# Performance work log

Measured on AMD Instinct MI355X. Metric: run time of the kernel, lower is better.

The kernel has to match this reference:

```python
import jax, jax.numpy as jnp
import numpy as np
import math

B, S, D, H = 2, 2048, 1024, 16
HD = D // H  # 64


def _rope(x, cos, sin):
    # x: [B,S,H,HD]; cos/sin: [S, HD//2]
    x2 = x.reshape(*x.shape[:-1], HD // 2, 2)
    x0, x1 = x2[..., 0], x2[..., 1]
    c = cos[None, :, None, :]
    s = sin[None, :, None, :]
    r0 = x0 * c - x1 * s
    r1 = x0 * s + x1 * c
    return jnp.stack([r0, r1], axis=-1).reshape(x.shape)


def setup_inputs() -> dict:
    key = jax.random.key(0)
    ks = jax.random.split(key, 6)
    x = jax.random.normal(ks[0], (B, S, D), dtype=jnp.float32)
    wq = jax.random.normal(ks[1], (D, D), dtype=jnp.float32) * 0.02
    wk = jax.random.normal(ks[2], (D, D), dtype=jnp.float32) * 0.02
    wv = jax.random.normal(ks[3], (D, D), dtype=jnp.float32) * 0.02
    wo = jax.random.normal(ks[4], (D, D), dtype=jnp.float32) * 0.02
    # standard RoPE frequencies: theta = 10000^(-2i/HD)
    inv_freq = 1.0 / (10000.0 ** (jnp.arange(0, HD, 2, dtype=jnp.float32) / HD))
    t = jnp.arange(S, dtype=jnp.float32)
    ang = t[:, None] * inv_freq[None, :]  # [S, HD//2]
    freqs_cos = jnp.cos(ang)
    freqs_sin = jnp.sin(ang)
    # causal additive mask [S, S]
    mask = jnp.where(jnp.tril(jnp.ones((S, S), dtype=bool)), 0.0, -1e9).astype(jnp.float32)
    return {"x": x, "wq": wq, "wk": wk, "wv": wv, "wo": wo,
            "freqs_cos": freqs_cos, "freqs_sin": freqs_sin, "mask": mask}


def reference(x, wq, wk, wv, wo, freqs_cos, freqs_sin, mask):
    b, s, d = x.shape
    # nn.Linear with no bias: y = x @ W^T
    q = jnp.einsum('bsd,od->bso', x, wq).reshape(b, s, H, HD)
    k = jnp.einsum('bsd,od->bso', x, wk).reshape(b, s, H, HD)
    v = jnp.einsum('bsd,od->bso', x, wv).reshape(b, s, H, HD)
    q = _rope(q, freqs_cos, freqs_sin)
    k = _rope(k, freqs_cos, freqs_sin)
    # [B,H,S,HD]
    q = q.transpose(0, 2, 1, 3)
    k = k.transpose(0, 2, 1, 3)
    v = v.transpose(0, 2, 1, 3)
    scores = jnp.einsum('bhqd,bhkd->bhqk', q, k) / math.sqrt(HD)
    scores = scores + mask[None, None, :, :]
    p = jax.nn.softmax(scores.astype(jnp.float32), axis=-1).astype(q.dtype)
    out = jnp.einsum('bhqk,bhkd->bhqd', p, v)
    out = out.transpose(0, 2, 1, 3).reshape(b, s, d)
    return jnp.einsum('bsd,od->bso', out, wo)
```

## Files before the change

### kernel.cpp

```cpp
#include <hip/hip_runtime.h>
#include <hip/hip_bf16.h>
#include <stdint.h>

#define NB 2
#define NS 2048
#define ND 1024
#define NH 16
#define NM (NB*NS)

typedef __attribute__((ext_vector_type(8))) short bf16x8;
typedef __attribute__((ext_vector_type(4))) float f32x4;

static __device__ __forceinline__ f32x4 mfma16(bf16x8 a, bf16x8 b, f32x4 c) {
  return __builtin_amdgcn_mfma_f32_16x16x32_bf16(a, b, c, 0, 0, 0);
}

static __device__ __forceinline__ void gload_lds16(const void* g, void* l) {
  __builtin_amdgcn_global_load_lds(
      (const __attribute__((address_space(1))) void*)g,
      (__attribute__((address_space(3))) void*)l, 16, 0, 0);
}

static __device__ __forceinline__ uint32_t pkbf2(float a, float b) {
  return (uint32_t)__bfloat16_as_ushort(__float2bfloat16(a)) |
         ((uint32_t)__bfloat16_as_ushort(__float2bfloat16(b)) << 16);
}

#define QSCALE 0.18033688011112042f

struct alignas(8) bh4 { __hip_bfloat16 x, y, z, w; };

__global__ void cvt_all(const float* __restrict__ x,
                        const float* __restrict__ w0, const float* __restrict__ w1,
                        const float* __restrict__ w2, const float* __restrict__ w3,
                        __hip_bfloat16* xb, __hip_bfloat16* o0, __hip_bfloat16* o1,
                        __hip_bfloat16* o2, __hip_bfloat16* o3) {
  const int b = blockIdx.x;
  const float* in;
  __hip_bfloat16* out;
  int i;
  if (b < 4096) { in = x; out = xb; i = b * 256 + threadIdx.x; }
  else {
    const int t = (b - 4096) >> 10;
    in  = (t == 0) ? w0 : (t == 1) ? w1 : (t == 2) ? w2 : w3;
    out = (t == 0) ? o0 : (t == 1) ? o1 : (t == 2) ? o2 : o3;
    i = ((b - 4096) & 1023) * 256 + threadIdx.x;
  }
  float4 v = reinterpret_cast<const float4*>(in)[i];
  bh4 o;
  o.x = __float2bfloat16(v.x);
  o.y = __float2bfloat16(v.y);
  o.z = __float2bfloat16(v.z);
  o.w = __float2bfloat16(v.w);
  reinterpret_cast<bh4*>(out)[i] = o;
}

__global__ __launch_bounds__(256) void gemm_qkv(
    const __hip_bfloat16* __restrict__ A,
    const __hip_bfloat16* __restrict__ Wq,
    const __hip_bfloat16* __restrict__ Wk,
    const __hip_bfloat16* __restrict__ Wv,
    const float* __restrict__ fcos,
    const float* __restrict__ fsin,
    __hip_bfloat16* __restrict__ Qo,
    __hip_bfloat16* __restrict__ Ko,
    __hip_bfloat16* __restrict__ Vo) {
  __shared__ __hip_bfloat16 sA[128 * 32];
  __shared__ __hip_bfloat16 sB[128 * 32];
  __shared__ __align__(16) char xtr[33792];

  const int wsel = blockIdx.y >> 3;
  const __hip_bfloat16* W = (wsel == 0) ? Wq : (wsel == 1) ? Wk : Wv;

  const int tid = threadIdx.x;
  const int wid = tid >> 6;
  const int lane = tid & 63;
  const int l4 = lane >> 4, l16 = lane & 15;
  const int brow = blockIdx.x * 128;
  const int bcol = (blockIdx.y & 7) * 128;
  const int wr = (wid >> 1) * 64;
  const int wc = (wid & 1) * 64;
  const int ss0 = brow & 2047;
  const int bbb = brow >> 11;

  if (wsel < 2) {
    float2* tab = (float2*)xtr;
#pragma unroll
    for (int i = 0; i < 4; ++i) {
      const int e = i * 1024 + tid * 4;
      const int ssl = e >> 5, p = e & 31;
      float4 c4 = *(const float4*)&fcos[(ss0 + ssl) * 32 + p];
      float4 s4 = *(const float4*)&fsin[(ss0 + ssl) * 32 + p];
      tab[ssl * 33 + p + 0] = {c4.x, s4.x};
      tab[ssl * 33 + p + 1] = {c4.y, s4.y};
      tab[ssl * 33 + p + 2] = {c4.z, s4.z};
      tab[ssl * 33 + p + 3] = {c4.w, s4.w};
    }
  }

  f32x4 acc[4][4] = {};

  const __hip_bfloat16* Ap = A + (size_t)(brow + (tid >> 2)) * 1024 + (tid & 3) * 8;
  const __hip_bfloat16* Wp = W + (size_t)(bcol + (tid >> 2)) * 1024 + (tid & 3) * 8;
  char* sAc = (char*)sA + wid * 1024;
  char* sBc = (char*)sB + wid * 1024;

  for (int kt = 0; kt < 32; ++kt) {
    const int k0 = kt * 32;
    __syncthreads();
    gload_lds16(Ap + k0,             sAc);
    gload_lds16(Ap + 64 * 1024 + k0, sAc + 4096);
    gload_lds16(Wp + k0,             sBc);
    gload_lds16(Wp + 64 * 1024 + k0, sBc + 4096);
    __syncthreads();

    bf16x8 af[4], bfr[4];
#pragma unroll
    for (int i = 0; i < 4; ++i)
      af[i] = *(const bf16x8*)&sA[(wr + i * 16 + l16) * 32 + l4 * 8];
#pragma unroll
    for (int i = 0; i < 4; ++i)
      bfr[i] = *(const bf16x8*)&sB[(wc + i * 16 + l16) * 32 + l4 * 8];
#pragma unroll
    for (int mi = 0; mi < 4; ++mi)
#pragma unroll
      for (int ni = 0; ni < 4; ++ni)
        acc[mi][ni] = mfma16(af[mi], bfr[ni], acc[mi][ni]);
  }

  if (wsel == 2) {
    __hip_bfloat16 (*tt)[132] = (__hip_bfloat16(*)[132])xtr;
#pragma unroll
    for (int h = 0; h < 2; ++h) {
      __syncthreads();
      if ((wid & 1) == h) {
#pragma unroll
        for (int mi = 0; mi < 4; ++mi)
#pragma unroll
          for (int ni = 0; ni < 4; ++ni) {
            const int c = ni * 16 + l16;
            const int r0 = wr + mi * 16 + l4 * 4;
            uint2 w;
            w.x = pkbf2(acc[mi][ni][0], acc[mi][ni][1]);
            w.y = pkbf2(acc[mi][ni][2], acc[mi][ni][3]);
            *(uint2*)&tt[c][r0] = w;
          }
      }
      __syncthreads();
      const int cl = tid >> 2;
      const int rq = (tid & 3) * 32;
      const int o = bcol + h * 64 + cl;
      const int hh = o >> 6, hd = o & 63;
      __hip_bfloat16* dst =
          Vo + ((size_t)(bbb * 16 + hh) * 64 + hd) * 2048 + ss0 + rq;
#pragma unroll
      for (int k2 = 0; k2 < 4; ++k2)
        *(uint4*)&dst[k2 * 8] = *(const uint4*)&tt[cl][rq + k2 * 8];
    }
  } else {
    const float2* tab = (const float2*)xtr;
    __hip_bfloat16* dst = (wsel == 0) ? Qo : Ko;
#pragma unroll
    for (int mi = 0; mi < 4; ++mi)
#pragma unroll
      for (int ni = 0; ni < 4; ++ni)
#pragma unroll
        for (int j = 0; j < 4; ++j) {
          float v = acc[mi][ni][j];
          const int rloc = wr + mi * 16 + l4 * 4 + j;
          const int col = bcol + wc + ni * 16 + l16;
          const int hh = col >> 6, hd = col & 63;
          float other = __shfl_xor(v, 1);
          const float2 cs = tab[rloc * 33 + (hd >> 1)];
          float r = (col & 1) ? (other * cs.y + v * cs.x)
                              : (v * cs.x - other * cs.y);
          if (wsel == 0) r *= QSCALE;
          dst[((size_t)(bbb * 16 + hh) * 2048 + ss0 + rloc) * 64 + hd] =
              __float2bfloat16(r);
        }
  }
}

__global__ __launch_bounds__(256) void gemm_out(
    const __hip_bfloat16* __restrict__ A,
    const __hip_bfloat16* __restrict__ W,
    float* __restrict__ C) {
  __shared__ __hip_bfloat16 sA[64 * 32];
  __shared__ __hip_bfloat16 sB[128 * 32];

  const int tid = threadIdx.x;
  const int wid = tid >> 6;
  const int lane = tid & 63;
  const int l4 = lane >> 4, l16 = lane & 15;
  const int brow = blockIdx.x * 64;
  const int bcol = blockIdx.y * 128;
  const int wr = (wid & 1) * 32;
  const int wc = (wid >> 1) * 64;

  f32x4 acc[2][4] = {};

  const __hip_bfloat16* Ap = A + (size_t)(brow + (tid >> 2)) * 1024 + (tid & 3) * 8;
  const __hip_bfloat16* Wp = W + (size_t)(bcol + (tid >> 2)) * 1024 + (tid & 3) * 8;
  char* sAc = (char*)sA + wid * 1024;
  char* sBc = (char*)sB + wid * 1024;

  for (int kt = 0; kt < 32; ++kt) {
    const int k0 = kt * 32;
    __syncthreads();
    gload_lds16(Ap + k0,             sAc);
    gload_lds16(Wp + k0,             sBc);
    gload_lds16(Wp + 64 * 1024 + k0, sBc + 4096);
    __syncthreads();

    bf16x8 af[2], bfr[4];
#pragma unroll
    for (int i = 0; i < 2; ++i)
      af[i] = *(const bf16x8*)&sA[(wr + i * 16 + l16) * 32 + l4 * 8];
#pragma unroll
    for (int i = 0; i < 4; ++i)
      bfr[i] = *(const bf16x8*)&sB[(wc + i * 16 + l16) * 32 + l4 * 8];
#pragma unroll
    for (int mi = 0; mi < 2; ++mi)
#pragma unroll
      for (int ni = 0; ni < 4; ++ni)
        acc[mi][ni] = mfma16(af[mi], bfr[ni], acc[mi][ni]);
  }

#pragma unroll
  for (int mi = 0; mi < 2; ++mi)
#pragma unroll
    for (int ni = 0; ni < 4; ++ni)
#pragma unroll
      for (int j = 0; j < 4; ++j) {
        const int row = brow + wr + mi * 16 + l4 * 4 + j;
        const int col = bcol + wc + ni * 16 + l16;
        C[(size_t)row * 1024 + col] = acc[mi][ni][j];
      }
}

__global__ __launch_bounds__(256) void attn_fwd(
    const __hip_bfloat16* __restrict__ Q,
    const __hip_bfloat16* __restrict__ K,
    const __hip_bfloat16* __restrict__ VT,
    __hip_bfloat16* __restrict__ AO) {
  const int L = blockIdx.x;
  int qt, bh;
  if (L < 256) { qt = 15 - (L >> 5); bh = L & 31; }
  else         { qt = (L >> 5) - 8;  bh = L & 31; }
  const int bb = bh >> 4;
  const int hh = bh & 15;
  const int tid = threadIdx.x;
  const int wid = tid >> 6;
  const int lane = tid & 63;
  const int l4 = lane >> 4, l16 = lane & 15;
  const int wq0 = qt * 128 + wid * 32;

  const __hip_bfloat16* Qg = Q + (size_t)bh * 2048 * 64;
  const __hip_bfloat16* Kg = K + (size_t)bh * 2048 * 64;
  const __hip_bfloat16* Vg = VT + (size_t)bh * 64 * 2048;

  __shared__ __hip_bfloat16 sP[4][32][72];

  bf16x8 qf[2][2];
#pragma unroll
  for (int q2 = 0; q2 < 2; ++q2)
#pragma unroll
    for (int dk = 0; dk < 2; ++dk)
      qf[q2][dk] = *(const bf16x8*)&Qg[(size_t)(wq0 + q2 * 16 + l16) * 64 + dk * 32 + l4 * 8];

  float lrun[2] = {0.f, 0.f};
  f32x4 oacc[2][4] = {};

  const int lastkv = (wq0 + 31) >> 6;
  for (int kv = 0; kv <= lastkv; ++kv) {
    const int kb = kv * 64;

    bf16x8 kfr[4][2];
#pragma unroll
    for (int kf = 0; kf < 4; ++kf)
#pragma unroll
      for (int dk = 0; dk < 2; ++dk)
        kfr[kf][dk] = *(const bf16x8*)&Kg[(size_t)(kb + kf * 16 + l16) * 64 + dk * 32 + l4 * 8];

    f32x4 sacc[4][2] = {};
    __builtin_amdgcn_s_setprio(1);
#pragma unroll
    for (int dk = 0; dk < 2; ++dk)
#pragma unroll
      for (int kf = 0; kf < 4; ++kf)
#pragma unroll
        for (int q2 = 0; q2 < 2; ++q2)
          sacc[kf][q2] = mfma16(kfr[kf][dk], qf[q2][dk], sacc[kf][q2]);
    __builtin_amdgcn_s_setprio(0);

    bf16x8 vfr[4][2];
#pragma unroll
    for (int df = 0; df < 4; ++df)
#pragma unroll
      for (int ks = 0; ks < 2; ++ks)
        vfr[df][ks] = *(const bf16x8*)&Vg[(size_t)(df * 16 + l16) * 2048 + kb + ks * 32 + l4 * 8];

    const bool need_mask = (kb + 63 > wq0);
#pragma unroll
    for (int q2 = 0; q2 < 2; ++q2) {
      const int qi = wq0 + q2 * 16 + l16;
      float pe[16];
#pragma unroll
      for (int kf = 0; kf < 4; ++kf)
#pragma unroll
        for (int j = 0; j < 4; ++j) {
          float s = sacc[kf][q2][j];
          if (need_mask && (kb + kf * 16 + l4 * 4 + j > qi)) s = -1e30f;
          pe[kf * 4 + j] = exp2f(s);
        }
#pragma unroll
      for (int kf = 0; kf < 4; ++kf) {
        uint2 w;
        w.x = pkbf2(pe[kf * 4 + 0], pe[kf * 4 + 1]);
        w.y = pkbf2(pe[kf * 4 + 2], pe[kf * 4 + 3]);
        *(uint2*)&sP[wid][q2 * 16 + l16][kf * 16 + l4 * 4] = w;
      }
      float ts = 0.f;
#pragma unroll
      for (int t = 0; t < 16; ++t) ts += pe[t];
      ts += __shfl_xor(ts, 16);
      ts += __shfl_xor(ts, 32);
      lrun[q2] += ts;
    }

    __builtin_amdgcn_s_setprio(1);
#pragma unroll
    for (int ks = 0; ks < 2; ++ks) {
      bf16x8 pfr[2];
#pragma unroll
      for (int mf = 0; mf < 2; ++mf)
        pfr[mf] = *(const bf16x8*)&sP[wid][mf * 16 + l16][ks * 32 + l4 * 8];
#pragma unroll
      for (int mf = 0; mf < 2; ++mf)
#pragma unroll
        for (int df = 0; df < 4; ++df)
          oacc[mf][df] = mfma16(pfr[mf], vfr[df][ks], oacc[mf][df]);
    }
    __builtin_amdgcn_s_setprio(0);
  }

  float inv[2];
#pragma unroll
  for (int q2 = 0; q2 < 2; ++q2) inv[q2] = 1.f / lrun[q2];
#pragma unroll
  for (int mf = 0; mf < 2; ++mf)
#pragma unroll
    for (int j = 0; j < 4; ++j) {
      const float ir = __shfl(inv[mf], l4 * 4 + j);
      const int ss = wq0 + mf * 16 + l4 * 4 + j;
#pragma unroll
      for (int df = 0; df < 4; ++df) {
        const int dd = hh * 64 + df * 16 + l16;
        AO[((size_t)bb * 2048 + ss) * 1024 + dd] =
            __float2bfloat16(oacc[mf][df][j] * ir);
      }
    }
}

extern "C" void kernel_launch(void* const* d_in, const int* in_sizes, int n_in,
                              void* d_out, int out_size, void* d_ws, size_t ws_size,
                              hipStream_t stream) {
  const float* x  = (const float*)d_in[0];
  const float* wq = (const float*)d_in[1];
  const float* wk = (const float*)d_in[2];
  const float* wv = (const float*)d_in[3];
  const float* wo = (const float*)d_in[4];
  const float* fc = (const float*)d_in[5];
  const float* fs = (const float*)d_in[6];

  char* ws = (char*)d_ws;
  const size_t MB = 1024 * 1024;
  __hip_bfloat16* xb  = (__hip_bfloat16*)(ws);
  __hip_bfloat16* wqb = (__hip_bfloat16*)(ws + 8 * MB);
  __hip_bfloat16* wkb = (__hip_bfloat16*)(ws + 10 * MB);
  __hip_bfloat16* wvb = (__hip_bfloat16*)(ws + 12 * MB);
  __hip_bfloat16* wob = (__hip_bfloat16*)(ws + 14 * MB);
  __hip_bfloat16* qws = (__hip_bfloat16*)(ws + 16 * MB);
  __hip_bfloat16* kws = (__hip_bfloat16*)(ws + 24 * MB);
  __hip_bfloat16* vws = (__hip_bfloat16*)(ws + 32 * MB);
  __hip_bfloat16* ao  = (__hip_bfloat16*)(ws + 40 * MB);

  cvt_all<<<8192, 256, 0, stream>>>(x, wq, wk, wv, wo, xb, wqb, wkb, wvb, wob);

  gemm_qkv<<<dim3(NM / 128, 24), 256, 0, stream>>>(xb, wqb, wkb, wvb, fc, fs,
                                                   qws, kws, vws);

  attn_fwd<<<dim3(512), 256, 0, stream>>>(qws, kws, vws, ao);

  gemm_out<<<dim3(NM / 64, ND / 128), 256, 0, stream>>>(ao, wob, (float*)d_out);
}
```

Before: 229.9 us.

## Double-buffer K/V tiles in LDS for attention and remap GEMM blocks across XCDs

```diff
diff --git a/kernel.cpp b/kernel.cpp
--- a/kernel.cpp
+++ b/kernel.cpp
@@ -69,15 +69,19 @@
   __shared__ __hip_bfloat16 sB[128 * 32];
   __shared__ __align__(16) char xtr[33792];
 
-  const int wsel = blockIdx.y >> 3;
+  const int bl = blockIdx.x;
+  const int logical = (bl & 7) * 96 + (bl >> 3);
+  const int xt = logical / 24;
+  const int yy = logical - xt * 24;
+  const int wsel = yy >> 3;
   const __hip_bfloat16* W = (wsel == 0) ? Wq : (wsel == 1) ? Wk : Wv;
 
   const int tid = threadIdx.x;
   const int wid = tid >> 6;
   const int lane = tid & 63;
   const int l4 = lane >> 4, l16 = lane & 15;
-  const int brow = blockIdx.x * 128;
-  const int bcol = (blockIdx.y & 7) * 128;
+  const int brow = xt * 128;
+  const int bcol = (yy & 7) * 128;
   const int wr = (wid >> 1) * 64;
   const int wc = (wid & 1) * 64;
   const int ss0 = brow & 2047;
@@ -188,12 +192,14 @@
   __shared__ __hip_bfloat16 sA[64 * 32];
   __shared__ __hip_bfloat16 sB[128 * 32];
 
+  const int bl = blockIdx.x;
+  const int logical = (bl & 7) * 64 + (bl >> 3);
   const int tid = threadIdx.x;
   const int wid = tid >> 6;
   const int lane = tid & 63;
   const int l4 = lane >> 4, l16 = lane & 15;
-  const int brow = blockIdx.x * 64;
-  const int bcol = blockIdx.y * 128;
+  const int brow = (logical >> 3) * 64;
+  const int bcol = (logical & 7) * 128;
   const int wr = (wid & 1) * 32;
   const int wc = (wid >> 1) * 64;
 
@@ -259,6 +265,8 @@
   const __hip_bfloat16* Kg = K + (size_t)bh * 2048 * 64;
   const __hip_bfloat16* Vg = VT + (size_t)bh * 64 * 2048;
 
+  __shared__ __align__(16) char sKb[2][8192];
+  __shared__ __align__(16) char sVb[2][8192];
   __shared__ __hip_bfloat16 sP[4][32][72];
 
   bf16x8 qf[2][2];
@@ -268,80 +276,107 @@
     for (int dk = 0; dk < 2; ++dk)
       qf[q2][dk] = *(const bf16x8*)&Qg[(size_t)(wq0 + q2 * 16 + l16) * 64 + dk * 32 + l4 * 8];
 
+  const int srow = lane >> 3;
+  const int scol = ((lane & 7) ^ srow) * 8;
+  const int fo0 = l16 * 128 + (((l4) ^ (l16 & 7)) * 16);
+  const int fo1 = l16 * 128 + (((4 + l4) ^ (l16 & 7)) * 16);
+
   float lrun[2] = {0.f, 0.f};
   f32x4 oacc[2][4] = {};
 
-  const int lastkv = (wq0 + 31) >> 6;
-  for (int kv = 0; kv <= lastkv; ++kv) {
+  const int nkv = 2 * qt + 2;
+
+#pragma unroll
+  for (int i = 0; i < 2; ++i) {
+    const int c = wid * 2 + i;
+    gload_lds16(Kg + (size_t)(c * 8 + srow) * 64 + scol,   &sKb[0][c * 1024]);
+    gload_lds16(Vg + (size_t)(c * 8 + srow) * 2048 + scol, &sVb[0][c * 1024]);
+  }
+
+  for (int kv = 0; kv < nkv; ++kv) {
+    const int cur = kv & 1;
     const int kb = kv * 64;
-
-    bf16x8 kfr[4][2];
-#pragma unroll
-    for (int kf = 0; kf < 4; ++kf)
+    __syncthreads();
+
+    if (kv + 1 < nkv) {
+      const int kb2 = kb + 64;
+#pragma unroll
+      for (int i = 0; i < 2; ++i) {
+        const int c = wid * 2 + i;
+        gload_lds16(Kg + (size_t)(kb2 + c * 8 + srow) * 64 + scol,   &sKb[cur ^ 1][c * 1024]);
+        gload_lds16(Vg + (size_t)(c * 8 + srow) * 2048 + kb2 + scol, &sVb[cur ^ 1][c * 1024]);
+      }
+    }
+
+    if (kb <= wq0 + 31) {
+      bf16x8 kfr[4][2];
+#pragma unroll
+      for (int kf = 0; kf < 4; ++kf) {
+        kfr[kf][0] = *(const bf16x8*)&sKb[cur][kf * 2048 + fo0];
+        kfr[kf][1] = *(const bf16x8*)&sKb[cur][kf * 2048 + fo1];
+      }
+
+      f32x4 sacc[4][2] = {};
+      __builtin_amdgcn_s_setprio(1);
 #pragma unroll
       for (int dk = 0; dk < 2; ++dk)
-        kfr[kf][dk] = *(const bf16x8*)&Kg[(size_t)(kb + kf * 16 + l16) * 64 + dk * 32 + l4 * 8];
-
-    f32x4 sacc[4][2] = {};
-    __builtin_amdgcn_s_setprio(1);
-#pragma unroll
-    for (int dk = 0; dk < 2; ++dk)
-#pragma unroll
-      for (int kf = 0; kf < 4; ++kf)
-#pragma unroll
-        for (int q2 = 0; q2 < 2; ++q2)
-          sacc[kf][q2] = mfma16(kfr[kf][dk], qf[q2][dk], sacc[kf][q2]);
-    __builtin_amdgcn_s_setprio(0);
-
-    bf16x8 vfr[4][2];
-#pragma unroll
-    for (int df = 0; df < 4; ++df)
-#pragma unroll
-      for (int ks = 0; ks < 2; ++ks)
-        vfr[df][ks] = *(const bf16x8*)&Vg[(size_t)(df * 16 + l16) * 2048 + kb + ks * 32 + l4 * 8];
-
-    const bool need_mask = (kb + 63 > wq0);
-#pragma unroll
-    for (int q2 = 0; q2 < 2; ++q2) {
-      const int qi = wq0 + q2 * 16 + l16;
-      float pe[16];
-#pragma unroll
-      for (int kf = 0; kf < 4; ++kf)
-#pragma unroll
-        for (int j = 0; j < 4; ++j) {
-          float s = sacc[kf][q2][j];
-          if (need_mask && (kb + kf * 16 + l4 * 4 + j > qi)) s = -1e30f;
-          pe[kf * 4 + j] = exp2f(s);
+#pragma unroll
+        for (int kf = 0; kf < 4; ++kf)
+#pragma unroll
+          for (int q2 = 0; q2 < 2; ++q2)
+            sacc[kf][q2] = mfma16(kfr[kf][dk], qf[q2][dk], sacc[kf][q2]);
+      __builtin_amdgcn_s_setprio(0);
+
+      bf16x8 vfr[4][2];
+#pragma unroll
+      for (int df = 0; df < 4; ++df) {
+        vfr[df][0] = *(const bf16x8*)&sVb[cur][df * 2048 + fo0];
+        vfr[df][1] = *(const bf16x8*)&sVb[cur][df * 2048 + fo1];
+      }
+
+      const bool need_mask = (kb + 63 > wq0);
+#pragma unroll
+      for (int q2 = 0; q2 < 2; ++q2) {
+        const int qi = wq0 + q2 * 16 + l16;
+        float pe[16];
+#pragma unroll
+        for (int kf = 0; kf < 4; ++kf)
+#pragma unroll
+          for (int j = 0; j < 4; ++j) {
+            float s = sacc[kf][q2][j];
+            if (need_mask && (kb + kf * 16 + l4 * 4 + j > qi)) s = -1e30f;
+            pe[kf * 4 + j] = exp2f(s);
+          }
+#pragma unroll
+        for (int kf = 0; kf < 4; ++kf) {
+          uint2 w;
+          w.x = pkbf2(pe[kf * 4 + 0], pe[kf * 4 + 1]);
+          w.y = pkbf2(pe[kf * 4 + 2], pe[kf * 4 + 3]);
+          *(uint2*)&sP[wid][q2 * 16 + l16][kf * 16 + l4 * 4] = w;
         }
-#pragma unroll
-      for (int kf = 0; kf < 4; ++kf) {
-        uint2 w;
-        w.x = pkbf2(pe[kf * 4 + 0], pe[kf * 4 + 1]);
-        w.y = pkbf2(pe[kf * 4 + 2], pe[kf * 4 + 3]);
-        *(uint2*)&sP[wid][q2 * 16 + l16][kf * 16 + l4 * 4] = w;
-      }
-      float ts = 0.f;
-#pragma unroll
-      for (int t = 0; t < 16; ++t) ts += pe[t];
-      ts += __shfl_xor(ts, 16);
-      ts += __shfl_xor(ts, 32);
-      lrun[q2] += ts;
+        float ts = 0.f;
+#pragma unroll
+        for (int t = 0; t < 16; ++t) ts += pe[t];
+        ts += __shfl_xor(ts, 16);
+        ts += __shfl_xor(ts, 32);
+        lrun[q2] += ts;
+      }
+
+      __builtin_amdgcn_s_setprio(1);
+#pragma unroll
+      for (int ks = 0; ks < 2; ++ks) {
+        bf16x8 pfr[2];
+#pragma unroll
+        for (int mf = 0; mf < 2; ++mf)
+          pfr[mf] = *(const bf16x8*)&sP[wid][mf * 16 + l16][ks * 32 + l4 * 8];
+#pragma unroll
+        for (int mf = 0; mf < 2; ++mf)
+#pragma unroll
+          for (int df = 0; df < 4; ++df)
+            oacc[mf][df] = mfma16(pfr[mf], vfr[df][ks], oacc[mf][df]);
+      }
+      __builtin_amdgcn_s_setprio(0);
     }
-
-    __builtin_amdgcn_s_setprio(1);
-#pragma unroll
-    for (int ks = 0; ks < 2; ++ks) {
-      bf16x8 pfr[2];
-#pragma unroll
-      for (int mf = 0; mf < 2; ++mf)
-        pfr[mf] = *(const bf16x8*)&sP[wid][mf * 16 + l16][ks * 32 + l4 * 8];
-#pragma unroll
-      for (int mf = 0; mf < 2; ++mf)
-#pragma unroll
-        for (int df = 0; df < 4; ++df)
-          oacc[mf][df] = mfma16(pfr[mf], vfr[df][ks], oacc[mf][df]);
-    }
-    __builtin_amdgcn_s_setprio(0);
   }
 
   float inv[2];
@@ -387,10 +422,9 @@
 
   cvt_all<<<8192, 256, 0, stream>>>(x, wq, wk, wv, wo, xb, wqb, wkb, wvb, wob);
 
-  gemm_qkv<<<dim3(NM / 128, 24), 256, 0, stream>>>(xb, wqb, wkb, wvb, fc, fs,
-                                                   qws, kws, vws);
+  gemm_qkv<<<768, 256, 0, stream>>>(xb, wqb, wkb, wvb, fc, fs, qws, kws, vws);
 
   attn_fwd<<<dim3(512), 256, 0, stream>>>(qws, kws, vws, ao);
 
-  gemm_out<<<dim3(NM / 64, ND / 128), 256, 0, stream>>>(ao, wob, (float*)d_out);
-}
+  gemm_out<<<512, 256, 0, stream>>>(ao, wob, (float*)d_out);
+}
```

Result: no change. 227.7 us (-1.0%).
